# Optimization experiments

Hardware: AMD Instinct MI355X
Metric: run time of the kernel (lower is better)

The kernel has to match this reference:

```python
import jax, jax.numpy as jnp
import numpy as np

NEG = -1e30  # effective -inf in fp32 log-space
BLANK = 0


def _rnnt_forward(pred_pad, target, pred_len, target_len):
    """RNNT loss (warp-rnnt semantics, gather=True, reduction='mean').

    pred_pad: [B, T, U+1, V] joint logits; target: [B, U] labels;
    pred_len, target_len: [B] valid lengths.
    """
    log_probs = jax.nn.log_softmax(pred_pad.astype(jnp.float32), axis=-1)
    B, T, U1, V = log_probs.shape
    U = U1 - 1
    blank_lp = log_probs[..., BLANK]                       # [B, T, U+1]
    # label emission log-prob at (t, u): P(target[u] | t, u), only for u < U
    label_lp = jnp.take_along_axis(
        log_probs[:, :, :U, :], target[:, None, :, None].astype(jnp.int32), axis=-1
    )[..., 0]                                              # [B, T, U]
    label_lp = jnp.pad(label_lp, ((0, 0), (0, 0), (0, 1)), constant_values=NEG)  # [B,T,U+1]

    def per_seq(blank, label):  # blank, label: [T, U+1]
        # alpha[0, u] = sum_{u'<u} label[0, u']
        row0 = jnp.concatenate([jnp.zeros((1,), jnp.float32),
                                jnp.cumsum(label[0, :-1])])

        def comb(x, y):
            a1, b1 = x
            a2, b2 = y
            return (a1 + a2, jnp.logaddexp(b2, b1 + a2))

        def step(prev_row, inp):
            blank_prev, label_t = inp            # blank[t-1], label[t]
            base = prev_row + blank_prev         # vertical (blank) transition
            # horizontal recurrence: row[u] = logaddexp(base[u], row[u-1] + label_t[u-1])
            a = jnp.concatenate([jnp.full((1,), NEG, jnp.float32), label_t[:-1]])
            _, row = jax.lax.associative_scan(comb, (a, base))
            return row, row

        _, rows = jax.lax.scan(step, row0, (blank[:-1], label[1:]))
        return jnp.concatenate([row0[None, :], rows], axis=0)  # [T, U+1]

    alphas = jax.vmap(per_seq)(blank_lp, label_lp)            # [B, T, U+1]
    b_idx = jnp.arange(B)
    t_idx = pred_len.astype(jnp.int32) - 1
    u_idx = target_len.astype(jnp.int32)
    ll = alphas[b_idx, t_idx, u_idx] + blank_lp[b_idx, t_idx, u_idx]
    return -jnp.mean(ll)


def setup_inputs() -> dict:
    key = jax.random.key(0)
    k1, k2, k3, k4 = jax.random.split(key, 4)
    B, T, U, V = 8, 128, 64, 1024
    pred_pad = jax.random.normal(k1, (B, T, U + 1, V), dtype=jnp.float32)
    target = jax.random.randint(k2, (B, U), 1, V, dtype=jnp.int32)  # avoid blank=0
    pred_len = jax.random.randint(k3, (B,), T // 2, T + 1, dtype=jnp.int32)
    target_len = jax.random.randint(k4, (B,), U // 2, U + 1, dtype=jnp.int32)
    return {"pred_pad": pred_pad, "target": target,
            "pred_len": pred_len, "target_len": target_len}


def reference(pred_pad, target, pred_len, target_len):
    return _rnnt_forward(pred_pad, target, pred_len, target_len)
```

## Files before the change

### kernel.cpp

```cpp
#include <hip/hip_runtime.h>

#define NEGF   (-1e30f)
#define T_DIM  128
#define U_DIM  64
#define U1     65
#define V_DIM  1024
#define B_DIM  8
#define DMAX   192
#define L2E    1.4426950408889634f
#define LN2    0.6931471805599453f

__device__ __forceinline__ float fexp2(float x) {
    float r; asm("v_exp_f32 %0, %1" : "=v"(r) : "v"(x)); return r;
}
__device__ __forceinline__ float flog2(float x) {
    float r; asm("v_log_f32 %0, %1" : "=v"(r) : "v"(x)); return r;
}

__global__ __launch_bounds__(256) void lse_kernel(
    const float* __restrict__ pred, const int* __restrict__ target,
    const int* __restrict__ pred_len, const int* __restrict__ target_len,
    float* __restrict__ pairF, float* __restrict__ out)
{
    if (blockIdx.x == 0 && threadIdx.x == 0) out[0] = 0.0f;

    const int wave = blockIdx.x * 4 + (threadIdx.x >> 6);
    const int lane = threadIdx.x & 63;
    const int b   = wave / (T_DIM * U1);
    const int rem = wave - b * (T_DIM * U1);
    const int t   = rem / U1;
    const int u   = rem - t * U1;

    if (t >= pred_len[b] || u > target_len[b]) return;

    const float*  row = pred + (size_t)wave * V_DIM;
    const float4* r4  = (const float4*)row;

    float4 a0 = r4[lane];
    float4 a1 = r4[lane + 64];
    float4 a2 = r4[lane + 128];
    float4 a3 = r4[lane + 192];

    float s = __expf(a0.x) + __expf(a0.y) + __expf(a0.z) + __expf(a0.w)
            + __expf(a1.x) + __expf(a1.y) + __expf(a1.z) + __expf(a1.w)
            + __expf(a2.x) + __expf(a2.y) + __expf(a2.z) + __expf(a2.w)
            + __expf(a3.x) + __expf(a3.y) + __expf(a3.z) + __expf(a3.w);
    #pragma unroll
    for (int off = 32; off; off >>= 1) s += __shfl_xor(s, off);

    const float l2s = flog2(s);

    float labv = 0.0f;
    if (u < U_DIM) {
        const int tg = target[b * U_DIM + u];
        const int g = tg >> 8, c = tg & 3, sl = (tg >> 2) & 63;
        float4 ag  = (g == 0) ? a0 : (g == 1) ? a1 : (g == 2) ? a2 : a3;
        float  cmp = (c == 0) ? ag.x : (c == 1) ? ag.y : (c == 2) ? ag.z : ag.w;
        labv = __shfl(cmp, sl);
    }

    if (lane == 0) {
        const int base = (b * DMAX + t + u) * U1;
        pairF[2 * (base + u)] = a0.x * L2E - l2s;
        if (u < U_DIM)
            pairF[2 * (base + u + 1) + 1] = labv * L2E - l2s;
    }
}

template<bool W64>
__device__ __forceinline__ float alpha_body(
    const float2* smem, const int u, const int d_end, const int uq)
{
    float cur = (u == 0) ? 0.0f : NEGF;
    float a64 = NEGF;

#define SLOT_DECL(K) float bl##K, lam##K, bl64##K, l63##K;
    SLOT_DECL(0) SLOT_DECL(1) SLOT_DECL(2) SLOT_DECL(3)
    SLOT_DECL(4) SLOT_DECL(5) SLOT_DECL(6) SLOT_DECL(7)

#define LOAD_SLOT(K, r) { \
        int rr = (r); if (rr > d_end) rr = d_end; \
        float2 a = smem[rr * U1 + u]; \
        bl##K  = (u <= rr) ? a.x : NEGF; \
        lam##K = ((unsigned)(u - 1) <= (unsigned)rr) ? a.y : NEGF; \
        if (W64) { \
            float2 qq = smem[rr * U1 + U_DIM]; \
            bl64##K = (rr >= U_DIM) ? qq.x : NEGF; \
            l63##K  = (rr >= 63)    ? qq.y : NEGF; \
        } else { bl64##K = NEGF; l63##K = NEGF; } \
    }

#define STEP(K) { \
        float h_pre = __int_as_float(__builtin_amdgcn_update_dpp( \
            0, __float_as_int(cur), 0x138 , 0xf, 0xf, true)); \
        float a63_ = W64 ? __int_as_float( \
            __builtin_amdgcn_readlane(__float_as_int(cur), 63)) : 0.0f; \
        float v = cur + bl##K; \
        float h = h_pre + lam##K; \
        float m = fmaxf(v, h); \
        cur = m + flog2(1.0f + fexp2(-fabsf(v - h))); \
        if (W64) { \
            float v2 = a64 + bl64##K; \
            float h2 = a63_ + l63##K; \
            float m2 = fmaxf(v2, h2); \
            a64 = m2 + flog2(1.0f + fexp2(-fabsf(v2 - h2))); \
        } \
    }

#define GROUP8 \
        STEP(0) LOAD_SLOT(0, db + 7)  \
        STEP(1) LOAD_SLOT(1, db + 8)  \
        STEP(2) LOAD_SLOT(2, db + 9)  \
        STEP(3) LOAD_SLOT(3, db + 10) \
        STEP(4) LOAD_SLOT(4, db + 11) \
        STEP(5) LOAD_SLOT(5, db + 12) \
        STEP(6) LOAD_SLOT(6, db + 13) \
        STEP(7) LOAD_SLOT(7, db + 14)

    LOAD_SLOT(0, 0) LOAD_SLOT(1, 1) LOAD_SLOT(2, 2) LOAD_SLOT(3, 3)
    LOAD_SLOT(4, 4) LOAD_SLOT(5, 5) LOAD_SLOT(6, 6) LOAD_SLOT(7, 7)

    int db = 1;
    for (; db + 7 <= d_end && db + 14 <= 62; db += 8) { GROUP8 }
    asm volatile("s_waitcnt vmcnt(0)" ::: "memory");
    for (; db + 7 <= d_end; db += 8) { GROUP8 }

    if (db + 0 <= d_end) STEP(0)
    if (db + 1 <= d_end) STEP(1)
    if (db + 2 <= d_end) STEP(2)
    if (db + 3 <= d_end) STEP(3)
    if (db + 4 <= d_end) STEP(4)
    if (db + 5 <= d_end) STEP(5)
    if (db + 6 <= d_end) STEP(6)

#undef GROUP8
#undef STEP
#undef LOAD_SLOT
#undef SLOT_DECL

    float val = W64 ? a64 : __shfl(cur, uq);
    float fb  = smem[d_end * U1 + uq].x;
    return (val + fb) * LN2;
}

__global__ __launch_bounds__(64) void alpha_kernel(
    const float* __restrict__ pairF,
    const int* __restrict__ pred_len, const int* __restrict__ target_len,
    float* __restrict__ out)
{
    __shared__ __align__(16) float2 smem[DMAX * U1 + 64];

    const int b  = blockIdx.x;
    const int u  = threadIdx.x;
    const int tl = pred_len[b];
    const int uq = target_len[b];
    const int d_end = tl - 1 + uq;

    const float* srcF = pairF + (size_t)b * (2 * DMAX * U1);

    const int niter = ((d_end + 1) * U1 + 127) >> 7;
    for (int i = 0; i < niter; ++i) {
        const float* g = srcF + (size_t)i * 256 + u * 4;
        __builtin_amdgcn_global_load_lds(
            (const __attribute__((address_space(1))) void*)g,
            (__attribute__((address_space(3))) void*)(&smem[i * 128]),
            16, 0, 0);
    }
    asm volatile("s_waitcnt vmcnt(16)" ::: "memory");

    float ll = (uq == U_DIM) ? alpha_body<true >(smem, u, d_end, uq)
                             : alpha_body<false>(smem, u, d_end, uq);

    if (u == 0) atomicAdd(out, -ll * (1.0f / B_DIM));
}

extern "C" void kernel_launch(void* const* d_in, const int* in_sizes, int n_in,
                              void* d_out, int out_size, void* d_ws, size_t ws_size,
                              hipStream_t stream) {
    const float* pred       = (const float*)d_in[0];
    const int*   target     = (const int*)d_in[1];
    const int*   pred_len   = (const int*)d_in[2];
    const int*   target_len = (const int*)d_in[3];
    float* out = (float*)d_out;

    float* pairF = (float*)d_ws;

    const int nrows = B_DIM * T_DIM * U1;
    lse_kernel<<<nrows / 4, 256, 0, stream>>>(pred, target, pred_len, target_len,
                                              pairF, out);
    alpha_kernel<<<B_DIM, 64, 0, stream>>>(pairF, pred_len, target_len, out);
}
```

Before: 38.39 us.

## Process two time rows per wave and stage LDS load waits progressively

The LSE kernel now has each wave handle two consecutive t rows at the same u. It issues eight float4 loads up front, which adds memory-level parallelism and halves the number of waves. The alpha kernel replaces the single early vmcnt(16) wait and the later vmcnt(0) with a ladder of vmcnt waits spread across the diagonal loop, so computation on early diagonals can start while later global-to-LDS loads are still in flight. The trade-offs are higher register pressure in the LSE kernel and a dependence on the exact count of outstanding loads in the wait thresholds.

```diff
diff --git a/kernel.cpp b/kernel.cpp
--- a/kernel.cpp
+++ b/kernel.cpp
@@ -26,44 +26,78 @@
 
     const int wave = blockIdx.x * 4 + (threadIdx.x >> 6);
     const int lane = threadIdx.x & 63;
-    const int b   = wave / (T_DIM * U1);
-    const int rem = wave - b * (T_DIM * U1);
-    const int t   = rem / U1;
-    const int u   = rem - t * U1;
-
-    if (t >= pred_len[b] || u > target_len[b]) return;
-
-    const float*  row = pred + (size_t)wave * V_DIM;
-    const float4* r4  = (const float4*)row;
-
-    float4 a0 = r4[lane];
-    float4 a1 = r4[lane + 64];
-    float4 a2 = r4[lane + 128];
-    float4 a3 = r4[lane + 192];
-
-    float s = __expf(a0.x) + __expf(a0.y) + __expf(a0.z) + __expf(a0.w)
-            + __expf(a1.x) + __expf(a1.y) + __expf(a1.z) + __expf(a1.w)
-            + __expf(a2.x) + __expf(a2.y) + __expf(a2.z) + __expf(a2.w)
-            + __expf(a3.x) + __expf(a3.y) + __expf(a3.z) + __expf(a3.w);
+    const int WPB  = (T_DIM / 2) * U1;
+    const int b    = wave / WPB;
+    const int rem  = wave - b * WPB;
+    const int tp   = rem / U1;
+    const int u    = rem - tp * U1;
+    const int t0   = tp * 2;
+
+    const int tl = pred_len[b], uq = target_len[b];
+    if (t0 >= tl || u > uq) return;
+    const bool has1 = (t0 + 1 < tl);
+
+    const float*  row0 = pred + ((size_t)(b * T_DIM + t0) * U1 + u) * V_DIM;
+    const float4* r40  = (const float4*)row0;
+    const float4* r41  = (const float4*)(row0 + (size_t)U1 * V_DIM);
+
+    float4 a0 = r40[lane];
+    float4 a1 = r40[lane + 64];
+    float4 a2 = r40[lane + 128];
+    float4 a3 = r40[lane + 192];
+    float4 c0, c1, c2, c3;
+    if (has1) {
+        c0 = r41[lane];
+        c1 = r41[lane + 64];
+        c2 = r41[lane + 128];
+        c3 = r41[lane + 192];
+    }
+
+    float s0 = __expf(a0.x) + __expf(a0.y) + __expf(a0.z) + __expf(a0.w)
+             + __expf(a1.x) + __expf(a1.y) + __expf(a1.z) + __expf(a1.w)
+             + __expf(a2.x) + __expf(a2.y) + __expf(a2.z) + __expf(a2.w)
+             + __expf(a3.x) + __expf(a3.y) + __expf(a3.z) + __expf(a3.w);
     #pragma unroll
-    for (int off = 32; off; off >>= 1) s += __shfl_xor(s, off);
-
-    const float l2s = flog2(s);
-
-    float labv = 0.0f;
+    for (int off = 32; off; off >>= 1) s0 += __shfl_xor(s0, off);
+    const float l2s0 = flog2(s0);
+
+    float l2s1 = 0.0f;
+    if (has1) {
+        float s1 = __expf(c0.x) + __expf(c0.y) + __expf(c0.z) + __expf(c0.w)
+                 + __expf(c1.x) + __expf(c1.y) + __expf(c1.z) + __expf(c1.w)
+                 + __expf(c2.x) + __expf(c2.y) + __expf(c2.z) + __expf(c2.w)
+                 + __expf(c3.x) + __expf(c3.y) + __expf(c3.z) + __expf(c3.w);
+        #pragma unroll
+        for (int off = 32; off; off >>= 1) s1 += __shfl_xor(s1, off);
+        l2s1 = flog2(s1);
+    }
+
+    float labv0 = 0.0f, labv1 = 0.0f;
     if (u < U_DIM) {
         const int tg = target[b * U_DIM + u];
         const int g = tg >> 8, c = tg & 3, sl = (tg >> 2) & 63;
         float4 ag  = (g == 0) ? a0 : (g == 1) ? a1 : (g == 2) ? a2 : a3;
-        float  cmp = (c == 0) ? ag.x : (c == 1) ? ag.y : (c == 2) ? ag.z : ag.w;
-        labv = __shfl(cmp, sl);
+        float  cm0 = (c == 0) ? ag.x : (c == 1) ? ag.y : (c == 2) ? ag.z : ag.w;
+        labv0 = __shfl(cm0, sl);
+        if (has1) {
+            float4 cg  = (g == 0) ? c0 : (g == 1) ? c1 : (g == 2) ? c2 : c3;
+            float  cm1 = (c == 0) ? cg.x : (c == 1) ? cg.y
+                       : (c == 2) ? cg.z : cg.w;
+            labv1 = __shfl(cm1, sl);
+        }
     }
 
     if (lane == 0) {
-        const int base = (b * DMAX + t + u) * U1;
-        pairF[2 * (base + u)] = a0.x * L2E - l2s;
+        const int base0 = (b * DMAX + t0 + u) * U1;
+        pairF[2 * (base0 + u)] = a0.x * L2E - l2s0;
         if (u < U_DIM)
-            pairF[2 * (base + u + 1) + 1] = labv * L2E - l2s;
+            pairF[2 * (base0 + u + 1) + 1] = labv0 * L2E - l2s0;
+        if (has1) {
+            const int base1 = base0 + U1;
+            pairF[2 * (base1 + u)] = c0.x * L2E - l2s1;
+            if (u < U_DIM)
+                pairF[2 * (base1 + u + 1) + 1] = labv1 * L2E - l2s1;
+        }
     }
 }
 
@@ -107,7 +141,7 @@
         } \
     }
 
-#define GROUP8 \
+#define GROUP8 { \
         STEP(0) LOAD_SLOT(0, db + 7)  \
         STEP(1) LOAD_SLOT(1, db + 8)  \
         STEP(2) LOAD_SLOT(2, db + 9)  \
@@ -115,15 +149,26 @@
         STEP(4) LOAD_SLOT(4, db + 11) \
         STEP(5) LOAD_SLOT(5, db + 12) \
         STEP(6) LOAD_SLOT(6, db + 13) \
-        STEP(7) LOAD_SLOT(7, db + 14)
-
+        STEP(7) LOAD_SLOT(7, db + 14) }
+
+#define WAITV(N) asm volatile("s_waitcnt vmcnt(" #N ")" ::: "memory");
+
+    WAITV(40)
     LOAD_SLOT(0, 0) LOAD_SLOT(1, 1) LOAD_SLOT(2, 2) LOAD_SLOT(3, 3)
     LOAD_SLOT(4, 4) LOAD_SLOT(5, 5) LOAD_SLOT(6, 6) LOAD_SLOT(7, 7)
 
     int db = 1;
-    for (; db + 7 <= d_end && db + 14 <= 62; db += 8) { GROUP8 }
-    asm volatile("s_waitcnt vmcnt(0)" ::: "memory");
-    for (; db + 7 <= d_end; db += 8) { GROUP8 }
+    for (; db + 7 <= d_end && db <= 1;  db += 8) GROUP8
+    WAITV(32)
+    for (; db + 7 <= d_end && db <= 17; db += 8) GROUP8
+    WAITV(24)
+    for (; db + 7 <= d_end && db <= 33; db += 8) GROUP8
+    WAITV(16)
+    for (; db + 7 <= d_end && db <= 49; db += 8) GROUP8
+    WAITV(8)
+    for (; db + 7 <= d_end && db <= 65; db += 8) GROUP8
+    WAITV(0)
+    for (; db + 7 <= d_end; db += 8) GROUP8
 
     if (db + 0 <= d_end) STEP(0)
     if (db + 1 <= d_end) STEP(1)
@@ -133,6 +178,7 @@
     if (db + 5 <= d_end) STEP(5)
     if (db + 6 <= d_end) STEP(6)
 
+#undef WAITV
 #undef GROUP8
 #undef STEP
 #undef LOAD_SLOT
@@ -166,7 +212,6 @@
             (__attribute__((address_space(3))) void*)(&smem[i * 128]),
             16, 0, 0);
     }
-    asm volatile("s_waitcnt vmcnt(16)" ::: "memory");
 
     float ll = (uq == U_DIM) ? alpha_body<true >(smem, u, d_end, uq)
                              : alpha_body<false>(smem, u, d_end, uq);
@@ -185,8 +230,8 @@
 
     float* pairF = (float*)d_ws;
 
-    const int nrows = B_DIM * T_DIM * U1;
-    lse_kernel<<<nrows / 4, 256, 0, stream>>>(pred, target, pred_len, target_len,
-                                              pairF, out);
+    const int nwaves = B_DIM * (T_DIM / 2) * U1;
+    lse_kernel<<<nwaves / 4, 256, 0, stream>>>(pred, target, pred_len,
+                                               target_len, pairF, out);
     alpha_kernel<<<B_DIM, 64, 0, stream>>>(pairF, pred_len, target_len, out);
 }
```

After: 38.89 us. About the same (+1.3%).

## Process eight rows per wave in LSE kernel with double-buffered prefetch

Applied to the files above, without the earlier changes.

Each wave in the log-softmax kernel now handles eight consecutive (t,u) rows instead of one. While it reduces the current row, it loads the next row into an alternate register set. The aim is to hide global-load latency and cut launch and wave scheduling overhead. The cost is more registers per wave and eight times fewer waves, which may lower the memory-level parallelism available to saturate bandwidth.

```diff
diff --git a/kernel.cpp b/kernel.cpp
--- a/kernel.cpp
+++ b/kernel.cpp
@@ -26,44 +26,80 @@
 
     const int wave = blockIdx.x * 4 + (threadIdx.x >> 6);
     const int lane = threadIdx.x & 63;
-    const int b   = wave / (T_DIM * U1);
-    const int rem = wave - b * (T_DIM * U1);
-    const int t   = rem / U1;
-    const int u   = rem - t * U1;
-
-    if (t >= pred_len[b] || u > target_len[b]) return;
-
-    const float*  row = pred + (size_t)wave * V_DIM;
-    const float4* r4  = (const float4*)row;
-
-    float4 a0 = r4[lane];
-    float4 a1 = r4[lane + 64];
-    float4 a2 = r4[lane + 128];
-    float4 a3 = r4[lane + 192];
-
-    float s = __expf(a0.x) + __expf(a0.y) + __expf(a0.z) + __expf(a0.w)
-            + __expf(a1.x) + __expf(a1.y) + __expf(a1.z) + __expf(a1.w)
-            + __expf(a2.x) + __expf(a2.y) + __expf(a2.z) + __expf(a2.w)
-            + __expf(a3.x) + __expf(a3.y) + __expf(a3.z) + __expf(a3.w);
+
+    const int r0 = wave * 8;
+    const int b  = r0 / (T_DIM * U1);
+    const int rem0 = r0 - b * (T_DIM * U1);
+    int t = rem0 / U1;
+    int u = rem0 - t * U1;
+
+    const int tl = pred_len[b], uq = target_len[b];
+    if (t >= tl) return;
+
+    const float* rowp = pred + (size_t)r0 * V_DIM;
+
+    float4 e0, e1, e2, e3, o0, o1, o2, o3;
+
+    {
+        const bool v = (u <= uq);
+        if (v) {
+            const float4* r4 = (const float4*)rowp;
+            e0 = r4[lane]; e1 = r4[lane + 64];
+            e2 = r4[lane + 128]; e3 = r4[lane + 192];
+        }
+    }
+
+    int tc = t, uc = u;
     #pragma unroll
-    for (int off = 32; off; off >>= 1) s += __shfl_xor(s, off);
-
-    const float l2s = flog2(s);
-
-    float labv = 0.0f;
-    if (u < U_DIM) {
-        const int tg = target[b * U_DIM + u];
-        const int g = tg >> 8, c = tg & 3, sl = (tg >> 2) & 63;
-        float4 ag  = (g == 0) ? a0 : (g == 1) ? a1 : (g == 2) ? a2 : a3;
-        float  cmp = (c == 0) ? ag.x : (c == 1) ? ag.y : (c == 2) ? ag.z : ag.w;
-        labv = __shfl(cmp, sl);
-    }
-
-    if (lane == 0) {
-        const int base = (b * DMAX + t + u) * U1;
-        pairF[2 * (base + u)] = a0.x * L2E - l2s;
-        if (u < U_DIM)
-            pairF[2 * (base + u + 1) + 1] = labv * L2E - l2s;
+    for (int i = 0; i < 8; ++i) {
+        int tn = tc, un = uc + 1;
+        if (un == U1) { un = 0; tn++; }
+
+        if (i < 7 && tn < tl && un <= uq) {
+            const float4* rn = (const float4*)(rowp + (size_t)(i + 1) * V_DIM);
+            if (i & 1) {
+                e0 = rn[lane]; e1 = rn[lane + 64];
+                e2 = rn[lane + 128]; e3 = rn[lane + 192];
+            } else {
+                o0 = rn[lane]; o1 = rn[lane + 64];
+                o2 = rn[lane + 128]; o3 = rn[lane + 192];
+            }
+        }
+
+        if (tc < tl && uc <= uq) {
+            const float4 a0 = (i & 1) ? o0 : e0;
+            const float4 a1 = (i & 1) ? o1 : e1;
+            const float4 a2 = (i & 1) ? o2 : e2;
+            const float4 a3 = (i & 1) ? o3 : e3;
+
+            float s = __expf(a0.x) + __expf(a0.y) + __expf(a0.z) + __expf(a0.w)
+                    + __expf(a1.x) + __expf(a1.y) + __expf(a1.z) + __expf(a1.w)
+                    + __expf(a2.x) + __expf(a2.y) + __expf(a2.z) + __expf(a2.w)
+                    + __expf(a3.x) + __expf(a3.y) + __expf(a3.z) + __expf(a3.w);
+            #pragma unroll
+            for (int off = 32; off; off >>= 1) s += __shfl_xor(s, off);
+            const float l2s = flog2(s);
+
+            float labv = 0.0f;
+            if (uc < U_DIM) {
+                const int tg = target[b * U_DIM + uc];
+                const int g = tg >> 8, c = tg & 3, sl = (tg >> 2) & 63;
+                float4 ag  = (g == 0) ? a0 : (g == 1) ? a1
+                           : (g == 2) ? a2 : a3;
+                float  cmp = (c == 0) ? ag.x : (c == 1) ? ag.y
+                           : (c == 2) ? ag.z : ag.w;
+                labv = __shfl(cmp, sl);
+            }
+
+            if (lane == 0) {
+                const int base = (b * DMAX + tc + uc) * U1;
+                pairF[2 * (base + uc)] = a0.x * L2E - l2s;
+                if (uc < U_DIM)
+                    pairF[2 * (base + uc + 1) + 1] = labv * L2E - l2s;
+            }
+        }
+
+        tc = tn; uc = un;
     }
 }
 
@@ -107,7 +143,7 @@
         } \
     }
 
-#define GROUP8 \
+#define GROUP8 { \
         STEP(0) LOAD_SLOT(0, db + 7)  \
         STEP(1) LOAD_SLOT(1, db + 8)  \
         STEP(2) LOAD_SLOT(2, db + 9)  \
@@ -115,15 +151,15 @@
         STEP(4) LOAD_SLOT(4, db + 11) \
         STEP(5) LOAD_SLOT(5, db + 12) \
         STEP(6) LOAD_SLOT(6, db + 13) \
-        STEP(7) LOAD_SLOT(7, db + 14)
+        STEP(7) LOAD_SLOT(7, db + 14) }
 
     LOAD_SLOT(0, 0) LOAD_SLOT(1, 1) LOAD_SLOT(2, 2) LOAD_SLOT(3, 3)
     LOAD_SLOT(4, 4) LOAD_SLOT(5, 5) LOAD_SLOT(6, 6) LOAD_SLOT(7, 7)
 
     int db = 1;
-    for (; db + 7 <= d_end && db + 14 <= 62; db += 8) { GROUP8 }
+    for (; db + 7 <= d_end && db + 14 <= 62; db += 8) GROUP8
     asm volatile("s_waitcnt vmcnt(0)" ::: "memory");
-    for (; db + 7 <= d_end; db += 8) { GROUP8 }
+    for (; db + 7 <= d_end; db += 8) GROUP8
 
     if (db + 0 <= d_end) STEP(0)
     if (db + 1 <= d_end) STEP(1)
@@ -185,8 +221,8 @@
 
     float* pairF = (float*)d_ws;
 
-    const int nrows = B_DIM * T_DIM * U1;
-    lse_kernel<<<nrows / 4, 256, 0, stream>>>(pred, target, pred_len, target_len,
-                                              pairF, out);
+    const int nblocks = (B_DIM * T_DIM * U1) / 8 / 4;
+    lse_kernel<<<nblocks, 256, 0, stream>>>(pred, target, pred_len, target_len,
+                                            pairF, out);
     alpha_kernel<<<B_DIM, 64, 0, stream>>>(pairF, pred_len, target_len, out);
 }
```

Measured after the change: 57.44 us. 49.6% more time.
